# Optimization experiments

Measured on AMD Instinct MI355X. Metric: run time of the kernel, lower is better.

The kernel has to match this reference:

```python
import jax, jax.numpy as jnp
import numpy as np

DIM = 1024
HEAD_DIM = 64
N_HEADS = DIM // HEAD_DIM  # 16
COND_DIM = 256
LENGTHS = (1, 4, 16, 64, 256, 1024)
SEQ = sum(LENGTHS)  # 1365
LN_EPS = 1e-5
ROT_D = 3 * (HEAD_DIM // 8)  # 24; 2*ROT_D = 48 <= HEAD_DIM


def _axial_pos(h, w):
    hp = np.linspace(-1.0, 1.0, h + 1); hp = (hp[:-1] + hp[1:]) / 2
    wp = np.linspace(-1.0, 1.0, w + 1); wp = (wp[:-1] + wp[1:]) / 2
    return np.stack(np.meshgrid(hp, wp, indexing='ij'), -1).reshape(h * w, 2)


def _make_theta():
    d = 5
    poses = []
    for i in range(d):
        pa = _axial_pos(32 >> i, 32 >> i)
        pr = np.full((pa.shape[0], 1), (d - i) / d)
        poses.insert(0, np.concatenate([pa, pr], -1))
    poses.insert(0, np.zeros((1, 3)))
    pos = np.concatenate(poses, 0)  # [1365, 3]
    log_min, log_max = np.log(np.pi), np.log(10 * np.pi)
    freqs = np.exp(np.linspace(log_min, log_max, HEAD_DIM // 8 * N_HEADS + 1)[:-1])
    freqs = freqs.reshape(HEAD_DIM // 8, N_HEADS).T  # [H, head_dim//8]
    th = pos[:, None, 0:1] * freqs  # [S, H, head_dim//8]
    tw = pos[:, None, 1:2] * freqs
    td = pos[:, None, 2:3] * freqs
    theta = np.concatenate([th, tw, td], -1)  # [S, H, ROT_D]
    return jnp.asarray(theta.transpose(1, 0, 2), dtype=jnp.float32)  # [H, S, ROT_D]


def _make_mask():
    m = np.zeros((SEQ, SEQ), dtype=bool)
    i = 0
    for L in LENGTHS:
        m[i:, i:i + L] = True
        i += L
    return jnp.asarray(m)


THETA = _make_theta()  # [H, S, ROT_D], constant buffer
MASK = _make_mask()    # [S, S] bool, constant buffer


def _rope(x, theta):
    # x: [B, H, S, head_dim]; theta: [H, S, ROT_D]
    d = theta.shape[-1]
    x1, x2, rest = x[..., :d], x[..., d:2 * d], x[..., 2 * d:]
    cos, sin = jnp.cos(theta), jnp.sin(theta)
    return jnp.concatenate([x1 * cos - x2 * sin, x2 * cos + x1 * sin, rest], -1)


def setup_inputs() -> dict:
    key = jax.random.key(0)
    ks = jax.random.split(key, 6)
    s = 0.02
    x = jax.random.normal(ks[0], (8, SEQ, DIM), jnp.float32)
    cond = jax.random.normal(ks[1], (8, 1, COND_DIM), jnp.float32)
    adaln_w = jax.random.normal(ks[2], (COND_DIM, 2 * DIM), jnp.float32) * s
    adaln_b = jnp.zeros((2 * DIM,), jnp.float32)
    qkv_w = jax.random.normal(ks[3], (DIM, 3 * DIM), jnp.float32) * s
    qkv_b = jnp.zeros((3 * DIM,), jnp.float32)
    out_w = jax.random.normal(ks[4], (DIM, DIM), jnp.float32) * s
    out_b = jnp.zeros((DIM,), jnp.float32)
    return {"x": x, "cond": cond, "adaln_w": adaln_w, "adaln_b": adaln_b,
            "qkv_w": qkv_w, "qkv_b": qkv_b, "out_w": out_w, "out_b": out_b}


def reference(x, cond, adaln_w, adaln_b, qkv_w, qkv_b, out_w, out_b):
    B, S, _ = x.shape
    skip = x
    # AdaLN: zero-init proj in the original; math is LN(x)*(w+1)+b
    wb = cond @ adaln_w + adaln_b  # [B, 1, 2*DIM]
    w, b = jnp.split(wb, 2, axis=-1)
    mu = x.mean(-1, keepdims=True)
    var = ((x - mu) ** 2).mean(-1, keepdims=True)
    xn = (x - mu) * jax.lax.rsqrt(var + LN_EPS)
    xn = xn * (w + 1.0) + b
    # QKV
    qkv = xn @ qkv_w + qkv_b  # [B, S, 3*DIM]
    qkv = qkv.reshape(B, S, 3, N_HEADS, HEAD_DIM).transpose(0, 3, 2, 1, 4)  # [B,H,3,S,hd]
    q, k, v = qkv[:, :, 0], qkv[:, :, 1], qkv[:, :, 2]
    theta = THETA[:, :S]  # [H, S, ROT_D]
    q = _rope(q, theta)
    k = _rope(k, theta)
    # block-causal masked SDPA
    scores = jnp.einsum('bhqd,bhkd->bhqk', q, k) / np.sqrt(HEAD_DIM).astype(np.float32)
    scores = jnp.where(MASK[:S, :S], scores, -1e30)
    attn = jax.nn.softmax(scores, axis=-1)
    o = jnp.einsum('bhqk,bhkd->bhqd', attn, v)
    o = o.transpose(0, 2, 1, 3).reshape(B, S, DIM)
    return o @ out_w + out_b + skip
```

## Files before the change

### kernel.cpp

```cpp
#include <hip/hip_runtime.h>
#include <math.h>


typedef unsigned short u16;
typedef unsigned short u16x8 __attribute__((ext_vector_type(8)));
typedef unsigned short u16x4 __attribute__((ext_vector_type(4)));
typedef __bf16        bf16x8 __attribute__((ext_vector_type(8)));
typedef float         f32x4  __attribute__((ext_vector_type(4)));

#define SEQ  1365
#define SP   1408
#define BHN  128
#define MTOT 10920
#define DIMN 1024
#define QSCALE 0.1803368801111204f

__device__ __forceinline__ u16 f2bf(float x){
  unsigned r; asm("v_cvt_pk_bf16_f32 %0, %1, %1" : "=v"(r) : "v"(x));
  return (u16)r;
}
__device__ __forceinline__ unsigned cvtpk(float a, float b){
  unsigned r; asm("v_cvt_pk_bf16_f32 %0, %1, %2" : "=v"(r) : "v"(a), "v"(b));
  return r;
}
__device__ __forceinline__ float bf2f(u16 b){
  return __builtin_bit_cast(float, ((unsigned)b) << 16);
}
__device__ __forceinline__ bf16x8 ldbf8(const u16* p){
  return __builtin_bit_cast(bf16x8, *(const u16x8*)p);
}
__device__ __forceinline__ bf16x8 ldsv(const char* p){
  return __builtin_bit_cast(bf16x8, *(const u16x8*)p);
}
__device__ __forceinline__ f32x4 mfma16(bf16x8 a, bf16x8 b, f32x4 c){
  return __builtin_amdgcn_mfma_f32_16x16x32_bf16(a, b, c, 0, 0, 0);
}
__device__ __forceinline__ void gload16(const u16* g, u16* l){
  __builtin_amdgcn_global_load_lds(
      (const __attribute__((address_space(1))) void*)(g),
      (__attribute__((address_space(3))) void*)(l), 16, 0, 0);
}

__global__ __launch_bounds__(256) void transpose_bf16(const float* __restrict__ in,
                                                      u16* __restrict__ outT,
                                                      int K, int N){
  __shared__ float tile[32][33];
  const int tx = threadIdx.x & 31, ty = threadIdx.x >> 5;
  const int n0 = blockIdx.x*32, k0 = blockIdx.y*32;
#pragma unroll
  for (int i=0;i<32;i+=8) tile[ty+i][tx] = in[(size_t)(k0+ty+i)*N + n0+tx];
  __syncthreads();
#pragma unroll
  for (int i=0;i<32;i+=8) outT[(size_t)(n0+ty+i)*K + k0+tx] = f2bf(tile[tx][ty+i]);
}

__global__ __launch_bounds__(256) void adaln_kernel(const float* __restrict__ cond,
                                                    const float* __restrict__ w,
                                                    const float* __restrict__ bsrc,
                                                    float* __restrict__ wb){
  __shared__ float cs[256];
  const int bt = blockIdx.x >> 3, ch = blockIdx.x & 7;
  const int t = threadIdx.x;
  cs[t] = cond[bt*256 + t];
  __syncthreads();
  const int n = ch*256 + t;
  float acc = bsrc[n];
  for (int j=0;j<256;j++) acc += cs[j] * w[(size_t)j*2048 + n];
  wb[bt*2048 + n] = acc;
}

__global__ __launch_bounds__(256) void theta_kernel(float* __restrict__ ctab,
                                                    float* __restrict__ stab){
  int idx = blockIdx.x*256 + threadIdx.x;
  if (idx >= 16*SEQ*24) return;
  int c = idx % 24;
  int rest = idx / 24;
  int s = rest % SEQ;
  int h = rest / SEQ;
  float p0 = 0.f, p1 = 0.f, p2 = 0.f;
  if (s >= 1){
    int start, sh; float pr;
    if      (s <   5){start=1;   sh=1; pr=0.2f;}
    else if (s <  21){start=5;   sh=2; pr=0.4f;}
    else if (s <  85){start=21;  sh=3; pr=0.6f;}
    else if (s < 341){start=85;  sh=4; pr=0.8f;}
    else             {start=341; sh=5; pr=1.0f;}
    int n = s - start;
    int row = n >> sh, colp = n & ((1<<sh)-1);
    float g = (float)(1 << sh);
    p0 = -1.f + (2*row+1)/g;
    p1 = -1.f + (2*colp+1)/g;
    p2 = pr;
  }
  int j = c & 7, comp = c >> 3;
  float kf = (float)(j*16 + h);
  float freq = 3.14159265358979323846f * exp2f(kf * (3.3219280948873623f/128.f));
  float pos = (comp==0) ? p0 : ((comp==1) ? p1 : p2);
  float th = pos * freq;
  ctab[idx] = cosf(th);
  stab[idx] = sinf(th);
}

__global__ __launch_bounds__(256) void ln_kernel(const float* __restrict__ x,
                                                 const float* __restrict__ wb,
                                                 u16* __restrict__ xn){
  const int row = blockIdx.x;
  const int b = row / SEQ;
  const int t = threadIdx.x, w = t>>6, l = t&63;
  const float4 v = ((const float4*)(x + (size_t)row*DIMN))[t];
  float s = v.x + v.y + v.z + v.w;
#pragma unroll
  for (int m=1; m<64; m<<=1) s += __shfl_xor(s, m);
  __shared__ float red1[4], red2[4];
  if (l == 0) red1[w] = s;
  __syncthreads();
  float mean = (red1[0]+red1[1]+red1[2]+red1[3]) * (1.f/1024.f);
  float dx = v.x-mean, dy = v.y-mean, dz = v.z-mean, dw = v.w-mean;
  float q = dx*dx + dy*dy + dz*dz + dw*dw;
#pragma unroll
  for (int m=1; m<64; m<<=1) q += __shfl_xor(q, m);
  if (l == 0) red2[w] = q;
  __syncthreads();
  float var = (red2[0]+red2[1]+red2[2]+red2[3]) * (1.f/1024.f);
  float rs = rsqrtf(var + 1e-5f);
  const float* wrow = wb + b*2048;
  int n0 = t*4;
  u16x4 o;
  o[0] = f2bf(dx*rs*(wrow[n0+0]+1.f) + wrow[1024+n0+0]);
  o[1] = f2bf(dy*rs*(wrow[n0+1]+1.f) + wrow[1024+n0+1]);
  o[2] = f2bf(dz*rs*(wrow[n0+2]+1.f) + wrow[1024+n0+2]);
  o[3] = f2bf(dw*rs*(wrow[n0+3]+1.f) + wrow[1024+n0+3]);
  *(u16x4*)&xn[(size_t)row*DIMN + n0] = o;
}

#define GSTAGE(dstA, dstB, koff)                                   \
  do {                                                             \
    _Pragma("unroll")                                              \
    for (int j_=0;j_<4;j_++) gload16(sA[j_]+(koff), (dstA)+j_*512);\
    _Pragma("unroll")                                              \
    for (int j_=0;j_<4;j_++) gload16(sB[j_]+(koff), (dstB)+j_*512);\
  } while(0)

__global__ __launch_bounds__(256, 2) void gemm_qkv(const u16* __restrict__ A,
                                                   const u16* __restrict__ BT,
                                                   const float* __restrict__ bias,
                                                   u16* __restrict__ qb, u16* __restrict__ kb,
                                                   u16* __restrict__ vb){
  __shared__ u16 SMEM[32768];
  u16* As0 = SMEM;        u16* As1 = SMEM + 8192;
  u16* Bs0 = SMEM + 16384; u16* Bs1 = SMEM + 24576;
  const int t = threadIdx.x, l = t & 63, w = t >> 6;
  const int lr = l & 15, lg = l >> 4;
  const int wr = w >> 1, wc = w & 1;

  const int bid = blockIdx.x;
  const int wg = (bid & 7)*264 + (bid >> 3);
  const int stile = wg/96, rr = wg - stile*96;
  const int mt = stile*4 + rr/24, nt = rr - (rr/24)*24;
  const int bat = mt / 11, mtl = mt - bat*11;
  const int s0 = mtl*128;
  const int bn = nt*128;

  const int row8 = l >> 3;
  const int gch  = (l & 7) ^ row8;
  const u16* sA[4]; const u16* sB[4];
#pragma unroll
  for (int j=0;j<4;j++){
    int srow = s0 + w*32 + j*8 + row8; if (srow > SEQ-1) srow = SEQ-1;
    sA[j] = A  + ((size_t)(bat*SEQ + srow))*1024 + gch*8;
    sB[j] = BT + (size_t)(bn + w*32 + j*8 + row8)*1024 + gch*8;
  }
  u16* dA0 = &As0[w*2048]; u16* dB0 = &Bs0[w*2048];
  u16* dA1 = &As1[w*2048]; u16* dB1 = &Bs1[w*2048];

  const int pch  = (lg ^ (lr & 7)) << 4;
  const int aoff = (wr*64 + lr)*128 + pch;
  const int boff = (wc*64 + lr)*128 + pch;

  f32x4 acc[4][4];
#pragma unroll
  for (int mi=0;mi<4;mi++)
#pragma unroll
    for (int ni=0;ni<4;ni++) acc[mi][ni] = (f32x4){0.f,0.f,0.f,0.f};

  GSTAGE(dA0, dB0, 0);
  GSTAGE(dA1, dB1, 64);
  asm volatile("s_waitcnt vmcnt(8)" ::: "memory");
  __builtin_amdgcn_s_barrier();
  __builtin_amdgcn_sched_barrier(0);

  for (int kt = 0; kt < 16; ++kt){
    const int bi = kt & 1;
    const char* Ab = (const char*)(bi ? As1 : As0);
    const char* Bb = (const char*)(bi ? Bs1 : Bs0);
    u16* dA = bi ? dA1 : dA0;
    u16* dB = bi ? dB1 : dB0;
    bf16x8 a0[4], b0[4], a1[4], b1[4];
#pragma unroll
    for (int mi=0;mi<4;mi++) a0[mi] = ldsv(Ab + (aoff + mi*2048));
#pragma unroll
    for (int ni=0;ni<4;ni++) b0[ni] = ldsv(Bb + (boff + ni*2048));
#pragma unroll
    for (int mi=0;mi<4;mi++) a1[mi] = ldsv(Ab + ((aoff + mi*2048) ^ 64));
#pragma unroll
    for (int ni=0;ni<4;ni++) b1[ni] = ldsv(Bb + ((boff + ni*2048) ^ 64));
    __builtin_amdgcn_s_setprio(1);
#pragma unroll
    for (int mi=0;mi<4;mi++)
#pragma unroll
      for (int ni=0;ni<4;ni++)
        acc[mi][ni] = mfma16(a0[mi], b0[ni], acc[mi][ni]);
    __builtin_amdgcn_s_setprio(0);
    asm volatile("s_waitcnt lgkmcnt(0)" ::: "memory");
    __builtin_amdgcn_s_barrier();
    __builtin_amdgcn_sched_barrier(0);
    if (kt < 14) GSTAGE(dA, dB, (kt+2)*64);
    __builtin_amdgcn_sched_barrier(0);
    __builtin_amdgcn_s_setprio(1);
#pragma unroll
    for (int mi=0;mi<4;mi++)
#pragma unroll
      for (int ni=0;ni<4;ni++)
        acc[mi][ni] = mfma16(a1[mi], b1[ni], acc[mi][ni]);
    __builtin_amdgcn_s_setprio(0);
    if (kt < 15){
      if (kt < 14) asm volatile("s_waitcnt vmcnt(8)" ::: "memory");
      else         asm volatile("s_waitcnt vmcnt(0)" ::: "memory");
      __builtin_amdgcn_s_barrier();
      __builtin_amdgcn_sched_barrier(0);
    }
  }

  __syncthreads();
  const int three = bn >> 10;
  const int hb = (bn & 1023) >> 6;
  if (three < 2){
    const float scl = (three==0) ? QSCALE : 1.0f;
#pragma unroll
    for (int mi=0;mi<4;mi++)
#pragma unroll
      for (int ni=0;ni<4;ni++){
        int col = wc*64 + ni*16 + lr;
        float bia = bias[bn + col];
#pragma unroll
        for (int r=0;r<4;r++){
          int ml = wr*64 + mi*16 + lg*4 + r;
          SMEM[ml*136 + col] = f2bf((acc[mi][ni][r] + bia) * scl);
        }
      }
    __syncthreads();
    u16* dst = (three==0) ? qb : kb;
    const int cs = t & 15, tm = t >> 4;
    const int h = hb + (cs>>3), d8 = (cs&7)*8;
#pragma unroll
    for (int p=0;p<8;p++){
      int ml = p*16 + tm;
      int s = s0 + ml;
      u16x8 vv = *(const u16x8*)&SMEM[ml*136 + cs*8];
      if (s < SEQ)
        *(u16x8*)&dst[((size_t)(bat*16 + h)*SP + s)*64 + d8] = vv;
    }
  } else {
#pragma unroll
    for (int mi=0;mi<4;mi++)
#pragma unroll
      for (int ni=0;ni<4;ni++){
        int col = wc*64 + ni*16 + lr;
        float bia = bias[bn + col];
#pragma unroll
        for (int r=0;r<4;r+=2){
          int ml = wr*64 + mi*16 + lg*4 + r;
          *(unsigned*)&SMEM[col*136 + ml] = cvtpk(acc[mi][ni][r]+bia, acc[mi][ni][r+1]+bia);
        }
      }
    __syncthreads();
    const int ss = t & 15, tdl = t >> 4;
    if (s0 + 127 < SEQ){
#pragma unroll
      for (int p=0;p<8;p++){
        int dl = p*16 + tdl;
        int h = hb + (dl>>6), d = dl & 63;
        u16x8 vv = *(const u16x8*)&SMEM[dl*136 + ss*8];
        *(u16x8*)&vb[((size_t)(bat*16 + h)*64 + d)*SP + s0 + ss*8] = vv;
      }
    } else {
#pragma unroll
      for (int p=0;p<8;p++){
        int dl = p*16 + tdl;
        int h = hb + (dl>>6), d = dl & 63;
        size_t rowb = ((size_t)(bat*16 + h)*64 + d)*SP;
#pragma unroll
        for (int j=0;j<8;j++){
          int s = s0 + ss*8 + j;
          if (s < SEQ) vb[rowb + s] = SMEM[dl*136 + ss*8 + j];
        }
      }
    }
  }
}

__global__ __launch_bounds__(256) void rope2_kernel(u16* __restrict__ qb,
                                                    u16* __restrict__ kb,
                                                    const float* __restrict__ ctab,
                                                    const float* __restrict__ stab){
  int rid = blockIdx.x*256 + threadIdx.x;
  if (rid >= BHN*SEQ) return;
  int bh = rid / SEQ, s = rid - bh*SEQ, h = bh & 15;
  const float* cp = ctab + (size_t)(h*SEQ + s)*24;
  const float* sp = stab + (size_t)(h*SEQ + s)*24;
  float cs[24], sn[24];
#pragma unroll
  for (int i=0;i<6;i++){
    ((float4*)cs)[i] = ((const float4*)cp)[i];
    ((float4*)sn)[i] = ((const float4*)sp)[i];
  }
  size_t base = ((size_t)bh*SP + s)*64;
  u16 buf[48];
#pragma unroll
  for (int i=0;i<6;i++) ((u16x8*)buf)[i] = *(const u16x8*)&qb[base + i*8];
#pragma unroll
  for (int j=0;j<24;j++){
    float x1 = bf2f(buf[j]), x2 = bf2f(buf[24+j]);
    buf[j]    = f2bf(x1*cs[j] - x2*sn[j]);
    buf[24+j] = f2bf(x2*cs[j] + x1*sn[j]);
  }
#pragma unroll
  for (int i=0;i<6;i++) *(u16x8*)&qb[base + i*8] = ((u16x8*)buf)[i];
#pragma unroll
  for (int i=0;i<6;i++) ((u16x8*)buf)[i] = *(const u16x8*)&kb[base + i*8];
#pragma unroll
  for (int j=0;j<24;j++){
    float x1 = bf2f(buf[j]), x2 = bf2f(buf[24+j]);
    buf[j]    = f2bf(x1*cs[j] - x2*sn[j]);
    buf[24+j] = f2bf(x2*cs[j] + x1*sn[j]);
  }
#pragma unroll
  for (int i=0;i<6;i++) *(u16x8*)&kb[base + i*8] = ((u16x8*)buf)[i];
}

__global__ __launch_bounds__(512, 2) void attn_kernel(const u16* __restrict__ qb,
                                                      const u16* __restrict__ kb,
                                                      const u16* __restrict__ vb,
                                                      u16* __restrict__ ob){
  __shared__ u16 Ks[2][4096];
  __shared__ u16 Vs[2][4096];
  __shared__ u16 Ps[256*72];
  const int bx = blockIdx.x;
  const int qt = (bx < 5) ? (bx + 1) : 0;
  const int bh = blockIdx.y;
  const int t = threadIdx.x, w = t>>6, l = t&63, lr = l&15, lg = l>>4, lg4 = lg<<2;
  const u16* qB = qb + (size_t)bh*SP*64;
  const u16* kB = kb + (size_t)bh*SP*64;
  const u16* vB = vb + (size_t)bh*64*SP;
  const int q0 = qt*256 + w*32;

  bf16x8 qf[2][2];
#pragma unroll
  for (int ni=0; ni<2; ni++){
    int qr = q0 + ni*16 + lr; if (qr > SEQ-1) qr = SEQ-1;
#pragma unroll
    for (int kk=0; kk<2; kk++)
      qf[ni][kk] = ldbf8(&qB[(size_t)qr*64 + kk*32 + lg*8]);
  }
  const int qg0 = q0 + lr, qg1 = q0 + 16 + lr;

  const int row8 = l >> 3;
  const int gch  = (l & 7) ^ row8;
  const u16* sK0 = kB + (size_t)(w*8 + row8)*64 + gch*8;
  const u16* sV0 = vB + (size_t)(w*8 + row8)*SP + gch*8;
  const int sw0 = ((lg)   ^ (lr & 7)) << 4;
  const int sw1 = ((4+lg) ^ (lr & 7)) << 4;

#define KVSTAGE(buf_, kb_)                              \
  do {                                                  \
    gload16(sK0 + (kb_)*64, &Ks[buf_][w*512]);          \
    gload16(sV0 + (kb_),    &Vs[buf_][w*512]);          \
  } while(0)

  f32x4 oacc[2][4];
#pragma unroll
  for (int mo=0;mo<2;mo++)
#pragma unroll
    for (int nd=0;nd<4;nd++) oacc[mo][nd] = (f32x4){0.f,0.f,0.f,0.f};
  float lst[2] = {0.f, 0.f};

  int qmax = min(qt*256+255, SEQ-1);
  int kend = (qmax<1)?1:(qmax<5)?5:(qmax<21)?21:(qmax<85)?85:(qmax<341)?341:SEQ;
  int nkt = (kend + 63) >> 6;

  KVSTAGE(0, 0);
  KVSTAGE(1, 64);

  for (int kt=0; kt<nkt; kt++){
    const int kbase = kt*64;
    const int cur = kt & 1;
    asm volatile("s_waitcnt vmcnt(2)" ::: "memory");
    __builtin_amdgcn_s_barrier();
    __builtin_amdgcn_sched_barrier(0);
    const char* Kb = (const char*)&Ks[cur][0];
    const char* Vb = (const char*)&Vs[cur][0];

    f32x4 sacc[4][2];
#pragma unroll
    for (int mi=0;mi<4;mi++){
      sacc[mi][0] = (f32x4){0.f,0.f,0.f,0.f};
      sacc[mi][1] = (f32x4){0.f,0.f,0.f,0.f};
    }
#pragma unroll
    for (int mi=0;mi<4;mi++){
      bf16x8 k0f = ldsv(Kb + (mi*16+lr)*128 + sw0);
      bf16x8 k1f = ldsv(Kb + (mi*16+lr)*128 + sw1);
      sacc[mi][0] = mfma16(k0f, qf[0][0], sacc[mi][0]);
      sacc[mi][0] = mfma16(k1f, qf[0][1], sacc[mi][0]);
      sacc[mi][1] = mfma16(k0f, qf[1][0], sacc[mi][1]);
      sacc[mi][1] = mfma16(k1f, qf[1][1], sacc[mi][1]);
    }

    int lastk = kbase + 63;
    int visLast = (lastk>=SEQ)?(1<<30):(lastk>=341)?341:(lastk>=85)?85:
                  (lastk>=21)?21:(lastk>=5)?5:(lastk>=1)?1:0;
    if (visLast > q0){
#pragma unroll
      for (int mi=0;mi<4;mi++){
        int kv = kbase + mi*16 + lg4;
#pragma unroll
        for (int r=0;r<4;r++){
          int key = kv + r;
          int visv = (key>=SEQ)?(1<<30):(key>=341)?341:(key>=85)?85:
                     (key>=21)?21:(key>=5)?5:(key>=1)?1:0;
          if (qg0 < visv) sacc[mi][0][r] = -1e30f;
          if (qg1 < visv) sacc[mi][1][r] = -1e30f;
        }
      }
    }

    float pa[2] = {0.f, 0.f}, pb[2] = {0.f, 0.f};
#pragma unroll
    for (int mi=0;mi<4;mi++)
#pragma unroll
      for (int ni=0;ni<2;ni++){
        float p0 = __builtin_amdgcn_exp2f(sacc[mi][ni][0]);
        float p1 = __builtin_amdgcn_exp2f(sacc[mi][ni][1]);
        float p2 = __builtin_amdgcn_exp2f(sacc[mi][ni][2]);
        float p3 = __builtin_amdgcn_exp2f(sacc[mi][ni][3]);
        pa[ni] += p0 + p1;
        pb[ni] += p2 + p3;
        uint2 pk = { cvtpk(p0, p1), cvtpk(p2, p3) };
        *(uint2*)&Ps[(w*32+ni*16+lr)*72 + mi*16 + lg4] = pk;
      }
#pragma unroll
    for (int ni=0;ni<2;ni++){
      float s = pa[ni] + pb[ni];
      s += __shfl_xor(s, 16);
      s += __shfl_xor(s, 32);
      lst[ni] += s;
    }

    bf16x8 pf[2][2];
#pragma unroll
    for (int mo=0;mo<2;mo++)
#pragma unroll
      for (int kk=0;kk<2;kk++)
        pf[mo][kk] = ldbf8(&Ps[(w*32+mo*16+lr)*72 + kk*32 + lg*8]);
#pragma unroll
    for (int nd=0;nd<4;nd++){
      bf16x8 v0 = ldsv(Vb + (nd*16+lr)*128 + sw0);
      bf16x8 v1 = ldsv(Vb + (nd*16+lr)*128 + sw1);
#pragma unroll
      for (int mo=0;mo<2;mo++){
        oacc[mo][nd] = mfma16(pf[mo][0], v0, oacc[mo][nd]);
        oacc[mo][nd] = mfma16(pf[mo][1], v1, oacc[mo][nd]);
      }
    }

    asm volatile("s_waitcnt lgkmcnt(0)" ::: "memory");
    __builtin_amdgcn_s_barrier();
    __builtin_amdgcn_sched_barrier(0);
    if (kt < nkt-1){
      int kpf = (kt+2 < nkt ? kt+2 : nkt-1)*64;
      KVSTAGE(cur, kpf);
    }
    __builtin_amdgcn_sched_barrier(0);
  }

  const int b = bh >> 4, h = bh & 15;
  float linv[2][4];
#pragma unroll
  for (int mo=0;mo<2;mo++)
#pragma unroll
    for (int r=0;r<4;r++)
      linv[mo][r] = 1.f / __shfl(lst[mo], lg4 + r);
#pragma unroll
  for (int mo=0;mo<2;mo++)
#pragma unroll
    for (int r=0;r<4;r++){
      int p = q0 + mo*16 + lg4 + r;
      if (p < SEQ){
#pragma unroll
        for (int nd=0;nd<4;nd++)
          ob[((size_t)(b*SEQ + p))*DIMN + h*64 + nd*16 + lr] = f2bf(oacc[mo][nd][r] * linv[mo][r]);
      }
    }
#undef KVSTAGE
}

__global__ __launch_bounds__(256, 2) void gemm_out(const u16* __restrict__ A,
                                                   const u16* __restrict__ BT,
                                                   const float* __restrict__ bias,
                                                   const float* __restrict__ skip,
                                                   float* __restrict__ out){
  __shared__ u16 SMEM[32768];
  u16* As0 = SMEM;        u16* As1 = SMEM + 8192;
  u16* Bs0 = SMEM + 16384; u16* Bs1 = SMEM + 24576;
  const int t = threadIdx.x, l = t & 63, w = t >> 6;
  const int lr = l & 15, lg = l >> 4;
  const int wr = w >> 1, wc = w & 1;

  const int bid = blockIdx.x;
  const int wg = (bid & 7)*88 + (bid >> 3);
  const int stile = wg/32, rr = wg & 31;
  const int mt = stile*4 + rr/8, nt = rr & 7;
  const int bat = mt / 11, mtl = mt - bat*11;
  const int s0 = mtl*128;
  const int bn = nt*128;

  const int row8 = l >> 3;
  const int gch  = (l & 7) ^ row8;
  const u16* sA[4]; const u16* sB[4];
#pragma unroll
  for (int j=0;j<4;j++){
    int srow = s0 + w*32 + j*8 + row8; if (srow > SEQ-1) srow = SEQ-1;
    sA[j] = A  + ((size_t)(bat*SEQ + srow))*1024 + gch*8;
    sB[j] = BT + (size_t)(bn + w*32 + j*8 + row8)*1024 + gch*8;
  }
  u16* dA0 = &As0[w*2048]; u16* dB0 = &Bs0[w*2048];
  u16* dA1 = &As1[w*2048]; u16* dB1 = &Bs1[w*2048];

  const int pch  = (lg ^ (lr & 7)) << 4;
  const int aoff = (wr*64 + lr)*128 + pch;
  const int boff = (wc*64 + lr)*128 + pch;

  f32x4 acc[4][4];
#pragma unroll
  for (int mi=0;mi<4;mi++)
#pragma unroll
    for (int ni=0;ni<4;ni++) acc[mi][ni] = (f32x4){0.f,0.f,0.f,0.f};

  GSTAGE(dA0, dB0, 0);
  GSTAGE(dA1, dB1, 64);
  asm volatile("s_waitcnt vmcnt(8)" ::: "memory");
  __builtin_amdgcn_s_barrier();
  __builtin_amdgcn_sched_barrier(0);

  for (int kt = 0; kt < 16; ++kt){
    const int bi = kt & 1;
    const char* Ab = (const char*)(bi ? As1 : As0);
    const char* Bb = (const char*)(bi ? Bs1 : Bs0);
    u16* dA = bi ? dA1 : dA0;
    u16* dB = bi ? dB1 : dB0;
    bf16x8 a0[4], b0[4], a1[4], b1[4];
#pragma unroll
    for (int mi=0;mi<4;mi++) a0[mi] = ldsv(Ab + (aoff + mi*2048));
#pragma unroll
    for (int ni=0;ni<4;ni++) b0[ni] = ldsv(Bb + (boff + ni*2048));
#pragma unroll
    for (int mi=0;mi<4;mi++) a1[mi] = ldsv(Ab + ((aoff + mi*2048) ^ 64));
#pragma unroll
    for (int ni=0;ni<4;ni++) b1[ni] = ldsv(Bb + ((boff + ni*2048) ^ 64));
    __builtin_amdgcn_s_setprio(1);
#pragma unroll
    for (int mi=0;mi<4;mi++)
#pragma unroll
      for (int ni=0;ni<4;ni++)
        acc[mi][ni] = mfma16(a0[mi], b0[ni], acc[mi][ni]);
    __builtin_amdgcn_s_setprio(0);
    asm volatile("s_waitcnt lgkmcnt(0)" ::: "memory");
    __builtin_amdgcn_s_barrier();
    __builtin_amdgcn_sched_barrier(0);
    if (kt < 14) GSTAGE(dA, dB, (kt+2)*64);
    __builtin_amdgcn_sched_barrier(0);
    __builtin_amdgcn_s_setprio(1);
#pragma unroll
    for (int mi=0;mi<4;mi++)
#pragma unroll
      for (int ni=0;ni<4;ni++)
        acc[mi][ni] = mfma16(a1[mi], b1[ni], acc[mi][ni]);
    __builtin_amdgcn_s_setprio(0);
    if (kt < 15){
      if (kt < 14) asm volatile("s_waitcnt vmcnt(8)" ::: "memory");
      else         asm volatile("s_waitcnt vmcnt(0)" ::: "memory");
      __builtin_amdgcn_s_barrier();
      __builtin_amdgcn_sched_barrier(0);
    }
  }

  __syncthreads();
  float* Lf = (float*)SMEM;
#pragma unroll
  for (int mi=0;mi<4;mi++)
#pragma unroll
    for (int ni=0;ni<4;ni++){
      int col = wc*64 + ni*16 + lr;
      float bia = bias[bn + col];
#pragma unroll
      for (int r=0;r<4;r++){
        int ml = wr*64 + mi*16 + lg*4 + r;
        Lf[ml*128 + col] = acc[mi][ni][r] + bia;
      }
    }
  __syncthreads();
  const int cs = t & 31, tm = t >> 5;
#pragma unroll
  for (int p=0;p<16;p++){
    int ml = p*8 + tm;
    int s = s0 + ml;
    if (s < SEQ){
      size_t idx2 = (size_t)(bat*SEQ + s)*1024 + bn + cs*4;
      float4 v4 = *(const float4*)&Lf[ml*128 + cs*4];
      const float4 sk = *(const float4*)&skip[idx2];
      float4 o4; o4.x=v4.x+sk.x; o4.y=v4.y+sk.y; o4.z=v4.z+sk.z; o4.w=v4.w+sk.w;
      *(float4*)&out[idx2] = o4;
    }
  }
}

extern "C" void kernel_launch(void* const* d_in, const int* in_sizes, int n_in,
                              void* d_out, int out_size, void* d_ws, size_t ws_size,
                              hipStream_t stream) {
  (void)in_sizes; (void)n_in; (void)out_size; (void)ws_size;
  const float* x        = (const float*)d_in[0];
  const float* cond     = (const float*)d_in[1];
  const float* adaln_w  = (const float*)d_in[2];
  const float* adaln_b  = (const float*)d_in[3];
  const float* qkv_w    = (const float*)d_in[4];
  const float* qkv_b    = (const float*)d_in[5];
  const float* out_w    = (const float*)d_in[6];
  const float* out_b    = (const float*)d_in[7];
  float* out = (float*)d_out;

  char* ws = (char*)d_ws;
  size_t off = 0;
  auto alloc = [&](size_t bytes)->void*{
    void* p = ws + off;
    off += (bytes + 255) & ~(size_t)255;
    return p;
  };
  float* wb     = (float*)alloc((size_t)8*2048*4);
  u16*   xn     = (u16*)  alloc((size_t)MTOT*DIMN*2);
  u16*   qkv_wT = (u16*)  alloc((size_t)3072*1024*2);
  u16*   out_wT = (u16*)  alloc((size_t)1024*1024*2);
  u16*   qbuf   = (u16*)  alloc((size_t)BHN*SP*64*2);
  u16*   kbuf   = (u16*)  alloc((size_t)BHN*SP*64*2);
  u16*   vbuf   = (u16*)  alloc((size_t)BHN*SP*64*2);
  float* ctab   = (float*)alloc((size_t)16*SEQ*24*4);
  float* stab   = (float*)alloc((size_t)16*SEQ*24*4);
  u16*   obuf   = xn;

  transpose_bf16<<<dim3(3072/32, 1024/32), 256, 0, stream>>>(qkv_w, qkv_wT, 1024, 3072);
  transpose_bf16<<<dim3(1024/32, 1024/32), 256, 0, stream>>>(out_w, out_wT, 1024, 1024);
  theta_kernel<<<(16*SEQ*24 + 255)/256, 256, 0, stream>>>(ctab, stab);
  adaln_kernel<<<64, 256, 0, stream>>>(cond, adaln_w, adaln_b, wb);
  ln_kernel<<<MTOT, 256, 0, stream>>>(x, wb, xn);
  gemm_qkv<<<2112, 256, 0, stream>>>(xn, qkv_wT, qkv_b, qbuf, kbuf, vbuf);
  rope2_kernel<<<(BHN*SEQ + 255)/256, 256, 0, stream>>>(qbuf, kbuf, ctab, stab);
  attn_kernel<<<dim3(6, BHN), 512, 0, stream>>>(qbuf, kbuf, vbuf, obuf);
  gemm_out<<<704, 256, 0, stream>>>(obuf, out_wT, out_b, x, out);
}
```

Before: 381.1 us.

## Feed softmax probabilities straight from registers into 16x16x16 MFMA, dropping LDS P staging

The attention kernel no longer writes the bf16 probability tile to shared memory and reads it back for the PV product. It relies on the score accumulator layout matching the A-operand layout of the 16x16x16 bf16 MFMA, so the packed probabilities go straight in as operands and V is read in 4-element chunks through the existing swizzle. Dropping the Ps buffer cuts LDS use, and launch bounds are raised to 6 blocks per CU to allow more occupancy. The trade-off is twice as many smaller MFMAs, more small LDS reads for V, and tighter register limits that may cause spills.

```diff
diff --git a/kernel.cpp b/kernel.cpp
--- a/kernel.cpp
+++ b/kernel.cpp
@@ -5,6 +5,7 @@
 typedef unsigned short u16;
 typedef unsigned short u16x8 __attribute__((ext_vector_type(8)));
 typedef unsigned short u16x4 __attribute__((ext_vector_type(4)));
+typedef short          s16x4 __attribute__((ext_vector_type(4)));
 typedef __bf16        bf16x8 __attribute__((ext_vector_type(8)));
 typedef float         f32x4  __attribute__((ext_vector_type(4)));
 
@@ -34,6 +35,9 @@
 }
 __device__ __forceinline__ f32x4 mfma16(bf16x8 a, bf16x8 b, f32x4 c){
   return __builtin_amdgcn_mfma_f32_16x16x32_bf16(a, b, c, 0, 0, 0);
+}
+__device__ __forceinline__ f32x4 mfma16k16(s16x4 a, s16x4 b, f32x4 c){
+  return __builtin_amdgcn_mfma_f32_16x16x16bf16_1k(a, b, c, 0, 0, 0);
 }
 __device__ __forceinline__ void gload16(const u16* g, u16* l){
   __builtin_amdgcn_global_load_lds(
@@ -338,13 +342,12 @@
   for (int i=0;i<6;i++) *(u16x8*)&kb[base + i*8] = ((u16x8*)buf)[i];
 }
 
-__global__ __launch_bounds__(512, 2) void attn_kernel(const u16* __restrict__ qb,
+__global__ __launch_bounds__(512, 6) void attn_kernel(const u16* __restrict__ qb,
                                                       const u16* __restrict__ kb,
                                                       const u16* __restrict__ vb,
                                                       u16* __restrict__ ob){
   __shared__ u16 Ks[2][4096];
   __shared__ u16 Vs[2][4096];
-  __shared__ u16 Ps[256*72];
   const int bx = blockIdx.x;
   const int qt = (bx < 5) ? (bx + 1) : 0;
   const int bh = blockIdx.y;
@@ -368,8 +371,10 @@
   const int gch  = (l & 7) ^ row8;
   const u16* sK0 = kB + (size_t)(w*8 + row8)*64 + gch*8;
   const u16* sV0 = vB + (size_t)(w*8 + row8)*SP + gch*8;
-  const int sw0 = ((lg)   ^ (lr & 7)) << 4;
-  const int sw1 = ((4+lg) ^ (lr & 7)) << 4;
+  const int lrm = lr & 7;
+  const int sw0 = ((lg)   ^ lrm) << 4;
+  const int sw1 = ((4+lg) ^ lrm) << 4;
+  const int vlo = (lg & 1) * 8;
 
 #define KVSTAGE(buf_, kb_)                              \
   do {                                                  \
@@ -435,6 +440,7 @@
     }
 
     float pa[2] = {0.f, 0.f}, pb[2] = {0.f, 0.f};
+    s16x4 paf[4][2];
 #pragma unroll
     for (int mi=0;mi<4;mi++)
 #pragma unroll
@@ -446,7 +452,7 @@
         pa[ni] += p0 + p1;
         pb[ni] += p2 + p3;
         uint2 pk = { cvtpk(p0, p1), cvtpk(p2, p3) };
-        *(uint2*)&Ps[(w*32+ni*16+lr)*72 + mi*16 + lg4] = pk;
+        paf[mi][ni] = __builtin_bit_cast(s16x4, pk);
       }
 #pragma unroll
     for (int ni=0;ni<2;ni++){
@@ -456,20 +462,15 @@
       lst[ni] += s;
     }
 
-    bf16x8 pf[2][2];
-#pragma unroll
-    for (int mo=0;mo<2;mo++)
-#pragma unroll
-      for (int kk=0;kk<2;kk++)
-        pf[mo][kk] = ldbf8(&Ps[(w*32+mo*16+lr)*72 + kk*32 + lg*8]);
 #pragma unroll
     for (int nd=0;nd<4;nd++){
-      bf16x8 v0 = ldsv(Vb + (nd*16+lr)*128 + sw0);
-      bf16x8 v1 = ldsv(Vb + (nd*16+lr)*128 + sw1);
-#pragma unroll
-      for (int mo=0;mo<2;mo++){
-        oacc[mo][nd] = mfma16(pf[mo][0], v0, oacc[mo][nd]);
-        oacc[mo][nd] = mfma16(pf[mo][1], v1, oacc[mo][nd]);
+#pragma unroll
+      for (int mi=0;mi<4;mi++){
+        int ch = (2*mi + (lg>>1)) ^ lrm;
+        s16x4 vf = __builtin_bit_cast(s16x4,
+            *(const uint2*)(Vb + (nd*16+lr)*128 + ch*16 + vlo));
+        oacc[0][nd] = mfma16k16(paf[mi][0], vf, oacc[0][nd]);
+        oacc[1][nd] = mfma16k16(paf[mi][1], vf, oacc[1][nd]);
       }
     }
 
```

Result: slower. 673.9 us (+76.8%).
